# Optimization experiments

Hardware: AMD Instinct MI355X
Metric: run time of the kernel (lower is better)

The kernel has to match this reference:

```python
import jax, jax.numpy as jnp
import numpy as np

B, T_ENC, T_DEC = 64, 256, 200
MEL, R = 80, 2
ENC_DIM = 256   # must equal attention_context_dim (context = weighted sum of encoder outputs)
ATT = 256       # attention_rnn_units == attention_context_dim
DEC = 256       # decoder_rnn_units
PRE1, PRE2 = 256, 128


def _gru(x, h, wih, whh, bih, bhh):
    # torch.nn.GRUCell math; weights are (3*H, in) torch layout
    gi = x @ wih.T + bih
    gh = h @ whh.T + bhh
    i_r, i_z, i_n = jnp.split(gi, 3, axis=-1)
    h_r, h_z, h_n = jnp.split(gh, 3, axis=-1)
    r = jax.nn.sigmoid(i_r + h_r)
    z = jax.nn.sigmoid(i_z + h_z)
    n = jnp.tanh(i_n + r * h_n)
    return (1.0 - z) * n + z * h


def setup_inputs() -> dict:
    key = jax.random.key(0)
    ks = iter(jax.random.split(key, 40))
    def nrm(shape, s=0.05):
        return jax.random.normal(next(ks), shape, dtype=jnp.float32) * s
    inp = {
        "encoder_outputs": nrm((B, T_ENC, ENC_DIM), 1.0),
        "inputs": nrm((B, T_DEC, MEL * R), 1.0),
        "memory_lengths": jax.random.randint(next(ks), (B,), T_ENC // 2, T_ENC + 1),
        # prenet
        "pre_w1": nrm((PRE1, MEL * R)), "pre_b1": jnp.zeros((PRE1,), jnp.float32),
        "pre_w2": nrm((PRE2, PRE1)),    "pre_b2": jnp.zeros((PRE2,), jnp.float32),
        # memory layer (no bias)
        "mem_w": nrm((ATT, ENC_DIM)),
        # attention GRUCell: input = prenet_out(128) + context(256)
        "att_wih": nrm((3 * ATT, PRE2 + ATT)), "att_whh": nrm((3 * ATT, ATT)),
        "att_bih": jnp.zeros((3 * ATT,), jnp.float32), "att_bhh": jnp.zeros((3 * ATT,), jnp.float32),
        # Bahdanau attention: query layer (no bias) and v vector
        "q_w": nrm((ATT, ATT)), "v_w": nrm((ATT,)),
        # project_to_decoder_in
        "proj_w": nrm((DEC, ATT + ATT)), "proj_b": jnp.zeros((DEC,), jnp.float32),
        # two decoder GRUCells
        "g1_wih": nrm((3 * DEC, DEC)), "g1_whh": nrm((3 * DEC, DEC)),
        "g1_bih": jnp.zeros((3 * DEC,), jnp.float32), "g1_bhh": jnp.zeros((3 * DEC,), jnp.float32),
        "g2_wih": nrm((3 * DEC, DEC)), "g2_whh": nrm((3 * DEC, DEC)),
        "g2_bih": jnp.zeros((3 * DEC,), jnp.float32), "g2_bhh": jnp.zeros((3 * DEC,), jnp.float32),
        # output projections
        "mel_w": nrm((MEL * R, DEC + ATT)), "mel_b": jnp.zeros((MEL * R,), jnp.float32),
        "stop_w": nrm((1, DEC + ATT)),      "stop_b": jnp.zeros((1,), jnp.float32),
    }
    return inp


def reference(encoder_outputs, inputs, memory_lengths,
              pre_w1, pre_b1, pre_w2, pre_b2, mem_w,
              att_wih, att_whh, att_bih, att_bhh, q_w, v_w,
              proj_w, proj_b,
              g1_wih, g1_whh, g1_bih, g1_bhh,
              g2_wih, g2_whh, g2_bih, g2_bhh,
              mel_w, mel_b, stop_w, stop_b):
    b = encoder_outputs.shape[0]
    processed_memory = encoder_outputs @ mem_w.T                    # (B,T_enc,ATT)
    pad_mask = jnp.arange(T_ENC)[None, :] >= memory_lengths[:, None]  # True = padding

    # teacher forcing: step t consumes previous target frame (zeros at t=0)
    x_seq = jnp.concatenate([jnp.zeros((b, 1, MEL * R), inputs.dtype), inputs[:, :-1]], axis=1)
    xs = jnp.swapaxes(x_seq, 0, 1)                                  # (T_dec,B,mel*r)

    def step(carry, x):
        h_att, ctx, h1, h2 = carry
        # prenet (dropout omitted: deterministic reference)
        pre = jax.nn.relu(jax.nn.relu(x @ pre_w1.T + pre_b1) @ pre_w2.T + pre_b2)
        # attention RNN
        h_att = _gru(jnp.concatenate([pre, ctx], -1), h_att, att_wih, att_whh, att_bih, att_bhh)
        # Bahdanau alignment
        score = jnp.einsum('btd,d->bt', jnp.tanh(processed_memory + (h_att @ q_w.T)[:, None, :]), v_w)
        score = jnp.where(pad_mask, -jnp.inf, score)
        align = jax.nn.softmax(score, axis=-1)                      # (B,T_enc)
        ctx = jnp.einsum('bt,btd->bd', align, encoder_outputs)      # (B,ATT)
        # decoder stack with residuals
        d = jnp.concatenate([h_att, ctx], -1) @ proj_w.T + proj_b
        h1 = _gru(d, h1, g1_wih, g1_whh, g1_bih, g1_bhh); d = h1 + d
        h2 = _gru(d, h2, g2_wih, g2_whh, g2_bih, g2_bhh); d = h2 + d
        p = jnp.concatenate([d, ctx], -1)
        mel = p @ mel_w.T + mel_b                                   # (B,mel*r)
        stop = jax.nn.sigmoid(p @ stop_w.T + stop_b)[:, 0]          # (B,)
        return (h_att, ctx, h1, h2), (mel, align, stop)

    zeros = lambda d: jnp.zeros((b, d), encoder_outputs.dtype)
    init = (zeros(ATT), zeros(ATT), zeros(DEC), zeros(DEC))
    _, (mels, aligns, stops) = jax.lax.scan(step, init, xs)

    mel_outputs = jnp.swapaxes(mels, 0, 1)                          # (B,T_dec,mel*r)
    attn_scores = jnp.swapaxes(aligns, 0, 1)                        # (B,T_dec,T_enc)
    stop_tokens = jnp.repeat(jnp.swapaxes(stops, 0, 1), R, axis=1)  # (B,T_dec*r)
    return mel_outputs, attn_scores, stop_tokens
```

## Files before the change

### kernel.cpp

```cpp
#include <hip/hip_runtime.h>
#include <math.h>
#include <stdint.h>

#define NB   64
#define TE   256
#define TD   200
#define MR   160

typedef _Float16 h2 __attribute__((ext_vector_type(2)));

__device__ __forceinline__ float dot2f(h2 a, h2 b, float c){
  return __builtin_amdgcn_fdot2(a, b, c, false);
}
__device__ __forceinline__ h2 u2h(unsigned int u){ return __builtin_bit_cast(h2, u); }
__device__ __forceinline__ unsigned int h2u(h2 h){ return __builtin_bit_cast(unsigned int, h); }
__device__ __forceinline__ unsigned f2u(float f){ return __builtin_bit_cast(unsigned, f); }
__device__ __forceinline__ float u2f(unsigned u){ return __builtin_bit_cast(float, u); }

__device__ __forceinline__ float sigmf(float x){
  return __fdividef(1.f, 1.f + __expf(-x));
}
__device__ __forceinline__ float tanhf_(float x){
  float ax = fabsf(x);
  float e  = __expf(-2.f*ax);
  float r  = __fdividef(1.f - e, 1.f + e);
  return copysignf(r, x);
}

static constexpr size_t OFF_PM   = 0;
static constexpr size_t OFF_ENCH = 8388608;
static constexpr size_t OFF_GIP  = 16777216;
static constexpr size_t OFF_P    = 36438016;
static constexpr size_t OFF_W2   = 49545216;
static constexpr size_t OFF_W8   = 50184192;
static constexpr size_t WS_NEEDED = 52936704;

static constexpr size_t A_PW1  = 0;
static constexpr size_t A_PW2  = 20480;
static constexpr size_t A_WIHP = 36864;
static constexpr size_t A_MEMW = 86016;
static constexpr size_t A_MELW = 118784;

static constexpr size_t B_ATTC = 0;
static constexpr size_t B_ATTH = 24576;
static constexpr size_t B_G1I  = 49152;
static constexpr size_t B_G1H  = 73728;
static constexpr size_t B_G2I  = 98304;
static constexpr size_t B_G2H  = 122880;
static constexpr size_t B_PROJ = 147456;
static constexpr size_t B_QW   = 163840;

__global__ void k_conv(const float* __restrict__ src, char* __restrict__ ws,
                       unsigned off_h2, int O, int Kh, int k0, int ld){
  int i = blockIdx.x*256 + threadIdx.x;
  if (i >= O*Kh) return;
  int o = i % O, kp = i / O;
  _Float16* dst = (_Float16*)(ws + OFF_W2) + 2*((size_t)off_h2 + i);
  dst[0] = (_Float16)src[(size_t)o*ld + k0 + 2*kp    ];
  dst[1] = (_Float16)src[(size_t)o*ld + k0 + 2*kp + 1];
}

__global__ void k_conv8(const float* __restrict__ src, char* __restrict__ ws,
                        unsigned off16, int O, int Kq, int k0, int ld){
  int i = blockIdx.x*256 + threadIdx.x;
  if (i >= O*Kq) return;
  int o = i % O, kq = i / O;
  const float* s = src + (size_t)o*ld + k0 + kq*8;
  h2 p0, p1, p2, p3;
  p0.x=(_Float16)s[0]; p0.y=(_Float16)s[1];
  p1.x=(_Float16)s[2]; p1.y=(_Float16)s[3];
  p2.x=(_Float16)s[4]; p2.y=(_Float16)s[5];
  p3.x=(_Float16)s[6]; p3.y=(_Float16)s[7];
  uint4 r; r.x=h2u(p0); r.y=h2u(p1); r.z=h2u(p2); r.w=h2u(p3);
  ((uint4*)(ws + OFF_W8))[(size_t)off16 + i] = r;
}

__global__ void k_pm(const float* __restrict__ enc, char* __restrict__ ws){
  int bt = blockIdx.x;
  int j  = threadIdx.x;
  const h2* mw = (const h2*)(ws + OFF_W2) + A_MEMW;
  _Float16* pmN  = (_Float16*)(ws + OFF_PM);
  _Float16* encH = (_Float16*)(ws + OFF_ENCH);
  __shared__ _Float16 e[256];
  float ev = enc[(size_t)bt*256 + j];
  e[j] = (_Float16)ev;
  encH[(size_t)bt*256 + j] = (_Float16)ev;
  __syncthreads();
  const h2* e2 = (const h2*)e;
  float acc = 0.f;
  #pragma unroll 8
  for (int kp=0; kp<128; ++kp) acc = dot2f(mw[kp*256 + j], e2[kp], acc);
  pmN[(size_t)bt*256 + j] = (_Float16)acc;
}

__global__ void k_pre(const float* __restrict__ xin, const float* __restrict__ b1,
                      const float* __restrict__ b2, const float* __restrict__ bih,
                      char* __restrict__ ws){
  int bt = blockIdx.x;
  int b = bt / TD, t = bt % TD;
  int j = threadIdx.x;
  const h2* w1 = (const h2*)(ws + OFF_W2) + A_PW1;
  const h2* w2 = (const h2*)(ws + OFF_W2) + A_PW2;
  const h2* wp = (const h2*)(ws + OFF_W2) + A_WIHP;
  _Float16* gip = (_Float16*)(ws + OFF_GIP) + (size_t)bt*768;
  __shared__ _Float16 xh[160];
  __shared__ _Float16 a1[256];
  __shared__ _Float16 pr[128];
  if (j < 160)
    xh[j] = (t==0) ? (_Float16)0.f : (_Float16)xin[((size_t)b*TD + (t-1))*MR + j];
  __syncthreads();
  {
    const h2* x2 = (const h2*)xh;
    float acc = b1[j];
    #pragma unroll 8
    for (int kp=0; kp<80; ++kp) acc = dot2f(w1[kp*256 + j], x2[kp], acc);
    a1[j] = (_Float16)fmaxf(acc, 0.f);
  }
  __syncthreads();
  if (j < 128){
    const h2* x2 = (const h2*)a1;
    float acc = b2[j];
    #pragma unroll 8
    for (int kp=0; kp<128; ++kp) acc = dot2f(w2[kp*128 + j], x2[kp], acc);
    pr[j] = (_Float16)fmaxf(acc, 0.f);
  }
  __syncthreads();
  {
    const h2* p2 = (const h2*)pr;
    for (int o=j; o<768; o+=256){
      float acc = bih[o];
      #pragma unroll 8
      for (int kp=0; kp<64; ++kp) acc = dot2f(wp[kp*768 + o], p2[kp], acc);
      gip[o] = (_Float16)acc;
    }
  }
}

__global__ void k_zero(float* __restrict__ out){
  int* prog = (int*)(out + (size_t)NB*TD*MR + (size_t)NB*TD*TE);
  if (threadIdx.x < 256) prog[threadIdx.x] = 0;
}

__device__ __forceinline__ float d4dot(uint4 w, uint4 x, float a){
  a = dot2f(u2h(w.x), u2h(x.x), a);
  a = dot2f(u2h(w.y), u2h(x.y), a);
  a = dot2f(u2h(w.z), u2h(x.z), a);
  a = dot2f(u2h(w.w), u2h(x.w), a);
  return a;
}

__device__ __forceinline__ void gemv4(const uint4* __restrict__ wI, const uint4* __restrict__ wH,
                                      const uint4* xI, const uint4* xH,
                                      int j, int ks, float* scr, int tid){
  float a0=0.f,a1=0.f,a2=0.f,a3=0.f;
  #pragma unroll 2
  for (int kq=ks*8; kq<ks*8+8; ++kq){
    uint4 xi = xI[kq];
    uint4 xh = xH[kq];
    a0 = d4dot(wI[kq*768 +       j], xi, a0);
    a1 = d4dot(wI[kq*768 + 256 + j], xi, a1);
    a2 = d4dot(wI[kq*768 + 512 + j], xi, a2);
    a0 = d4dot(wH[kq*768 +       j], xh, a0);
    a1 = d4dot(wH[kq*768 + 256 + j], xh, a1);
    a3 = d4dot(wH[kq*768 + 512 + j], xh, a3);
  }
  float* r = scr + tid*4;
  r[0]=a0; r[1]=a1; r[2]=a2; r[3]=a3;
}

__global__ __launch_bounds__(1024) void k_dec(
    const int*   __restrict__ memlen,
    const float* __restrict__ att_bhh,
    const float* __restrict__ vw,
    const float* __restrict__ proj_b,
    const float* __restrict__ g1_bih, const float* __restrict__ g1_bhh,
    const float* __restrict__ g2_bih, const float* __restrict__ g2_bhh,
    float* __restrict__ out, char* __restrict__ ws)
{
  const int tid  = threadIdx.x;
  const int x    = blockIdx.x;
  const int y    = x >> 3;
  const int role = y & 3;
  const int b    = ((y >> 2) << 3) | (x & 7);
  const int ks   = tid >> 8;
  const int j    = tid & 255;

  const uint4* W8 = (const uint4*)(ws + OFF_W8);
  int* prog = (int*)(out + (size_t)NB*TD*MR + (size_t)NB*TD*TE);
  int* pP   = prog;
  int* pAl  = prog + 64;
  int* pD   = prog + 128;
  int* pB1  = prog + 192;
  unsigned* gX = (unsigned*)((_Float16*)(ws + OFF_GIP) + (size_t)b*TD*768);
  unsigned* uSlot = (unsigned*)out + (size_t)NB*TD*128 + (size_t)b*768;
  unsigned* aSlot = (unsigned*)out + (size_t)NB*TD*128 + (size_t)NB*768 + (size_t)b*256;

  __shared__ __align__(16) _Float16 hAh[256], ctxh[256], hh[256], dh[256];
  __shared__ float hAf[256], hf[256], df[256];
  __shared__ float qf[256], sc[256], al[256], vl[256];
  __shared__ float scr[4096];
  __shared__ float red2[4];
  __shared__ __align__(16) uint4 pmL[8192];

  if (role == 0){
    const uint4* wAH = W8 + B_ATTH;
    const uint4* wQ4 = W8 + B_QW;
    const uint4* pm4 = (const uint4*)(ws + OFF_PM) + (size_t)b*8192;
    const _Float16* gipB = (const _Float16*)(ws + OFF_GIP) + (size_t)b*TD*768;
    float* outA = out + (size_t)NB*TD*MR + (size_t)b*TD*TE;
    const int ml = memlen[b];

    for (int idx = tid; idx < 8192; idx += 1024){
      int tp = idx >> 5, g = idx & 31;
      pmL[(tp<<5) | (g ^ (tp & 7))] = pm4[idx];
    }
    if (tid < 256){ hAh[tid]=(_Float16)0.f; hAf[tid]=0.f; vl[tid]=vw[tid]; }
    __syncthreads();
    const uint4* hA4 = (const uint4*)hAh;

    #pragma unroll 1
    for (int t=0; t<TD; ++t){
      float a0=0.f, a1=0.f, a3=0.f;
      #pragma unroll 2
      for (int i=0;i<8;++i){
        int kq = ks*8+i;
        uint4 xv = hA4[kq];
        a0 = d4dot(wAH[kq*768 +       j], xv, a0);
        a1 = d4dot(wAH[kq*768 + 256 + j], xv, a1);
        a3 = d4dot(wAH[kq*768 + 512 + j], xv, a3);
      }
      { float* r = scr + tid*3; r[0]=a0; r[1]=a1; r[2]=a3; }
      if (t > 0 && tid==0){
        while (__hip_atomic_load(pP+b, __ATOMIC_RELAXED, __HIP_MEMORY_SCOPE_AGENT) < t)
          __builtin_amdgcn_s_sleep(1);
      }
      __syncthreads();
      if (tid < 256){
        const _Float16* gp = gipB + (size_t)t*768;
        float s0 = scr[tid*3+0]+scr[(256+tid)*3+0]+scr[(512+tid)*3+0]+scr[(768+tid)*3+0];
        float s1 = scr[tid*3+1]+scr[(256+tid)*3+1]+scr[(512+tid)*3+1]+scr[(768+tid)*3+1];
        float s3 = scr[tid*3+2]+scr[(256+tid)*3+2]+scr[(512+tid)*3+2]+scr[(768+tid)*3+2];
        float s2 = 0.f;
        if (t > 0){
          s0 += u2f(__hip_atomic_load(uSlot +       tid, __ATOMIC_RELAXED, __HIP_MEMORY_SCOPE_AGENT));
          s1 += u2f(__hip_atomic_load(uSlot + 256 + tid, __ATOMIC_RELAXED, __HIP_MEMORY_SCOPE_AGENT));
          s2  = u2f(__hip_atomic_load(uSlot + 512 + tid, __ATOMIC_RELAXED, __HIP_MEMORY_SCOPE_AGENT));
        }
        float r = sigmf(s0 + (float)gp[tid]     + att_bhh[tid]);
        float z = sigmf(s1 + (float)gp[256+tid] + att_bhh[256+tid]);
        float n = tanhf_(s2 + (float)gp[512+tid] + r*(s3 + att_bhh[512+tid]));
        float h = (1.f-z)*n + z*hAf[tid];
        hAf[tid]=h; hAh[tid]=(_Float16)h;
      }
      __syncthreads();
      { float a=0.f;
        #pragma unroll 2
        for (int kq=ks*8; kq<ks*8+8; ++kq)
          a = d4dot(wQ4[kq*256 + j], hA4[kq], a);
        scr[tid]=a; }
      if (tid<128)
        __hip_atomic_store(gX + (size_t)t*384 + tid, ((const unsigned*)hAh)[tid],
                           __ATOMIC_RELAXED, __HIP_MEMORY_SCOPE_AGENT);
      __syncthreads();
      if (tid<256) qf[tid] = scr[tid]+scr[256+tid]+scr[512+tid]+scr[768+tid];
      __syncthreads();
      { float s=0.f;
        #pragma unroll
        for (int i=0;i<8;++i){
          int g = ks*8 + i;
          uint4 q4 = pmL[(j<<5) | (g ^ (j&7))];
          int d0 = ks*64 + i*8;
          h2 p0=u2h(q4.x), p1=u2h(q4.y), p2=u2h(q4.z), p3=u2h(q4.w);
          s += vl[d0+0]*tanhf_((float)p0.x + qf[d0+0]);
          s += vl[d0+1]*tanhf_((float)p0.y + qf[d0+1]);
          s += vl[d0+2]*tanhf_((float)p1.x + qf[d0+2]);
          s += vl[d0+3]*tanhf_((float)p1.y + qf[d0+3]);
          s += vl[d0+4]*tanhf_((float)p2.x + qf[d0+4]);
          s += vl[d0+5]*tanhf_((float)p2.y + qf[d0+5]);
          s += vl[d0+6]*tanhf_((float)p3.x + qf[d0+6]);
          s += vl[d0+7]*tanhf_((float)p3.y + qf[d0+7]);
        }
        scr[tid]=s; }
      __syncthreads();
      if (tid<256){
        float s = scr[tid]+scr[256+tid]+scr[512+tid]+scr[768+tid];
        float e = (tid < ml) ? __expf(s) : 0.f;
        sc[tid] = e;
        float sv = e;
        #pragma unroll
        for (int o=32;o>0;o>>=1) sv += __shfl_down(sv,o,64);
        if ((tid&63)==0) red2[tid>>6]=sv;
      }
      __syncthreads();
      if (tid<256){
        float sum = red2[0]+red2[1]+red2[2]+red2[3];
        float a = sc[tid]*__fdividef(1.f,sum);
        outA[(size_t)t*TE + tid]=a;
        __hip_atomic_store(aSlot + tid, f2u(a),
                           __ATOMIC_RELAXED, __HIP_MEMORY_SCOPE_AGENT);
      }
      __syncthreads();
      if (tid==0)
        __hip_atomic_store(pAl+b, t+1, __ATOMIC_RELEASE, __HIP_MEMORY_SCOPE_AGENT);
    }
  } else if (role == 1){
    const uint4* wAC  = W8 + B_ATTC;
    const uint4* wPRJ = W8 + B_PROJ;
    const unsigned* encW = (const unsigned*)(ws + OFF_ENCH) + (size_t)b*TE*128;
    _Float16* pstB = (_Float16*)(ws + OFF_P) + (size_t)b*TD*512;
    unsigned* encL = (unsigned*)pmL;
    const uint4* hA4  = (const uint4*)hAh;
    const uint4* ctx4 = (const uint4*)ctxh;
    const int tsl = tid>>7, dp = tid&127;

    for (int idx = tid; idx < 32768; idx += 1024) encL[idx] = encW[idx];
    __syncthreads();

    #pragma unroll 1
    for (int t=0; t<TD; ++t){
      if (tid==0){
        while (__hip_atomic_load(pAl+b, __ATOMIC_RELAXED, __HIP_MEMORY_SCOPE_AGENT) < t+1)
          __builtin_amdgcn_s_sleep(1);
      }
      __syncthreads();
      if (tid<256)
        al[tid] = u2f(__hip_atomic_load(aSlot + tid, __ATOMIC_RELAXED, __HIP_MEMORY_SCOPE_AGENT));
      if (tid >= 256 && tid < 384)
        ((unsigned*)hAh)[tid-256] = __hip_atomic_load(gX + (size_t)t*384 + (tid-256),
                                                      __ATOMIC_RELAXED, __HIP_MEMORY_SCOPE_AGENT);
      __syncthreads();
      { float c0=0.f, c1=0.f;
        #pragma unroll 8
        for (int tp=tsl*32; tp<tsl*32+32; ++tp){
          float a = al[tp];
          h2 e = u2h(encL[tp*128 + dp]);
          c0 += a*(float)e.x; c1 += a*(float)e.y;
        }
        scr[tid*2]=c0; scr[tid*2+1]=c1; }
      __syncthreads();
      if (tid<128){
        float c0=0.f, c1=0.f;
        #pragma unroll
        for (int k=0;k<8;++k){ c0 += scr[(k*128+tid)*2]; c1 += scr[(k*128+tid)*2+1]; }
        h2 c; c.x=(_Float16)c0; c.y=(_Float16)c1;
        unsigned w = h2u(c);
        ((unsigned*)ctxh)[tid] = w;
        ((unsigned*)pstB)[(size_t)t*256 + 128 + tid] = w;
      }
      __syncthreads();
      { float a0=0.f, a1=0.f, a2=0.f;
        #pragma unroll 2
        for (int kq=ks*8; kq<ks*8+8; ++kq){
          uint4 xv = ctx4[kq];
          a0 = d4dot(wAC[kq*768 +       j], xv, a0);
          a1 = d4dot(wAC[kq*768 + 256 + j], xv, a1);
          a2 = d4dot(wAC[kq*768 + 512 + j], xv, a2);
        }
        float* r = scr + tid*3; r[0]=a0; r[1]=a1; r[2]=a2; }
      __syncthreads();
      if (tid<256){
        float p0 = scr[tid*3+0]+scr[(256+tid)*3+0]+scr[(512+tid)*3+0]+scr[(768+tid)*3+0];
        float p1 = scr[tid*3+1]+scr[(256+tid)*3+1]+scr[(512+tid)*3+1]+scr[(768+tid)*3+1];
        float p2 = scr[tid*3+2]+scr[(256+tid)*3+2]+scr[(512+tid)*3+2]+scr[(768+tid)*3+2];
        __hip_atomic_store(uSlot +       tid, f2u(p0), __ATOMIC_RELAXED, __HIP_MEMORY_SCOPE_AGENT);
        __hip_atomic_store(uSlot + 256 + tid, f2u(p1), __ATOMIC_RELAXED, __HIP_MEMORY_SCOPE_AGENT);
        __hip_atomic_store(uSlot + 512 + tid, f2u(p2), __ATOMIC_RELAXED, __HIP_MEMORY_SCOPE_AGENT);
      }
      __syncthreads();
      if (tid==0)
        __hip_atomic_store(pP+b, t+1, __ATOMIC_RELEASE, __HIP_MEMORY_SCOPE_AGENT);
      { float a=0.f;
        #pragma unroll 2
        for (int kq=ks*16; kq<ks*16+16; ++kq){
          uint4 xa = (kq < 32) ? hA4[kq] : ctx4[kq-32];
          a = d4dot(wPRJ[kq*256 + j], xa, a);
        }
        scr[tid]=a; }
      __syncthreads();
      if (tid<128){
        const int o0 = 2*tid, o1 = o0+1;
        float d0 = scr[o0]+scr[256+o0]+scr[512+o0]+scr[768+o0] + proj_b[o0];
        float d1 = scr[o1]+scr[256+o1]+scr[512+o1]+scr[768+o1] + proj_b[o1];
        h2 p; p.x=(_Float16)d0; p.y=(_Float16)d1;
        __hip_atomic_store(gX + (size_t)t*384 + 256 + tid, h2u(p),
                           __ATOMIC_RELAXED, __HIP_MEMORY_SCOPE_AGENT);
      }
      __syncthreads();
      if (tid==0)
        __hip_atomic_store(pD+b, t+1, __ATOMIC_RELEASE, __HIP_MEMORY_SCOPE_AGENT);
    }
  } else {
    const bool isB1 = (role == 2);
    const uint4* wI = W8 + (isB1 ? B_G1I : B_G2I);
    const uint4* wH = W8 + (isB1 ? B_G1H : B_G2H);
    const float* bih = isB1 ? g1_bih : g2_bih;
    const float* bhh = isB1 ? g1_bhh : g2_bhh;
    int* pin = isB1 ? pD : pB1;
    unsigned* oX = (unsigned*)out + (size_t)b*TD*128;
    const unsigned* inP = isB1 ? (gX + 256) : oX;
    const int instr = isB1 ? 384 : 128;
    _Float16* pstB = (_Float16*)(ws + OFF_P) + (size_t)b*TD*512;

    if (tid<256){ hh[tid]=(_Float16)0.f; hf[tid]=0.f; }
    __syncthreads();
    const uint4* h4  = (const uint4*)hh;
    const uint4* dd4 = (const uint4*)dh;

    #pragma unroll 1
    for (int t=0; t<TD; ++t){
      if (tid==0){
        while (__hip_atomic_load(pin+b, __ATOMIC_RELAXED, __HIP_MEMORY_SCOPE_AGENT) < t+1)
          __builtin_amdgcn_s_sleep(1);
      }
      __syncthreads();
      if (tid<128){
        unsigned w = __hip_atomic_load(inP + (size_t)t*instr + tid,
                                       __ATOMIC_RELAXED, __HIP_MEMORY_SCOPE_AGENT);
        ((unsigned*)dh)[tid] = w;
        h2 p = u2h(w);
        df[2*tid]   = (float)p.x;
        df[2*tid+1] = (float)p.y;
      }
      __syncthreads();
      gemv4(wI, wH, dd4, h4, j, ks, scr, tid);
      __syncthreads();
      if (tid<256){
        float s0 = scr[tid*4+0]+scr[(256+tid)*4+0]+scr[(512+tid)*4+0]+scr[(768+tid)*4+0];
        float s1 = scr[tid*4+1]+scr[(256+tid)*4+1]+scr[(512+tid)*4+1]+scr[(768+tid)*4+1];
        float s2 = scr[tid*4+2]+scr[(256+tid)*4+2]+scr[(512+tid)*4+2]+scr[(768+tid)*4+2];
        float s3 = scr[tid*4+3]+scr[(256+tid)*4+3]+scr[(512+tid)*4+3]+scr[(768+tid)*4+3];
        float r = sigmf(s0 + bih[tid]     + bhh[tid]);
        float z = sigmf(s1 + bih[256+tid] + bhh[256+tid]);
        float n = tanhf_(s2 + bih[512+tid] + r*(s3 + bhh[512+tid]));
        float h = (1.f-z)*n + z*hf[tid];
        float dn = h + df[tid];
        hf[tid]=h; hh[tid]=(_Float16)h;
        dh[tid]=(_Float16)dn;
        if (!isB1) pstB[(size_t)t*512 + tid] = (_Float16)dn;
      }
      __syncthreads();
      if (isB1){
        if (tid<128)
          __hip_atomic_store(oX + (size_t)t*128 + tid, ((const unsigned*)dh)[tid],
                             __ATOMIC_RELAXED, __HIP_MEMORY_SCOPE_AGENT);
        __syncthreads();
        if (tid==0)
          __hip_atomic_store(pB1+b, t+1, __ATOMIC_RELEASE, __HIP_MEMORY_SCOPE_AGENT);
      }
    }
  }
}

__global__ void k_post(const float* __restrict__ mel_b, const float* __restrict__ stop_w,
                       const float* __restrict__ stop_b, float* __restrict__ out,
                       char* __restrict__ ws){
  int bt = blockIdx.x;
  int b = bt / TD, t = bt % TD;
  int j = threadIdx.x;
  const h2* wm = (const h2*)(ws + OFF_W2) + A_MELW;
  const _Float16* p = (const _Float16*)(ws + OFF_P) + (size_t)bt*512;
  __shared__ _Float16 pl[512];
  ((uint32_t*)pl)[j] = ((const uint32_t*)p)[j];
  __syncthreads();
  const h2* p2 = (const h2*)pl;
  if (j < 160){
    float acc = mel_b[j];
    #pragma unroll 8
    for (int kp=0; kp<256; ++kp) acc = dot2f(wm[kp*160 + j], p2[kp], acc);
    out[(size_t)bt*MR + j] = acc;
  } else if (j == 160){
    float acc = stop_b[0];
    for (int k=0; k<512; ++k) acc += stop_w[k]*(float)pl[k];
    float s = __fdividef(1.f, 1.f + __expf(-acc));
    float* os = out + (size_t)NB*TD*MR + (size_t)NB*TD*TE + (size_t)b*2*TD;
    os[2*t]   = s;
    os[2*t+1] = s;
  }
}

extern "C" void kernel_launch(void* const* d_in, const int* in_sizes, int n_in,
                              void* d_out, int out_size, void* d_ws, size_t ws_size,
                              hipStream_t stream)
{
  const float* enc     = (const float*)d_in[0];
  const float* xin     = (const float*)d_in[1];
  const int*   mlen    = (const int*)  d_in[2];
  const float* pre_w1  = (const float*)d_in[3];
  const float* pre_b1  = (const float*)d_in[4];
  const float* pre_w2  = (const float*)d_in[5];
  const float* pre_b2  = (const float*)d_in[6];
  const float* mem_w   = (const float*)d_in[7];
  const float* att_wih = (const float*)d_in[8];
  const float* att_whh = (const float*)d_in[9];
  const float* att_bih = (const float*)d_in[10];
  const float* att_bhh = (const float*)d_in[11];
  const float* q_w     = (const float*)d_in[12];
  const float* v_w     = (const float*)d_in[13];
  const float* proj_w  = (const float*)d_in[14];
  const float* proj_b  = (const float*)d_in[15];
  const float* g1_wih  = (const float*)d_in[16];
  const float* g1_whh  = (const float*)d_in[17];
  const float* g1_bih  = (const float*)d_in[18];
  const float* g1_bhh  = (const float*)d_in[19];
  const float* g2_wih  = (const float*)d_in[20];
  const float* g2_whh  = (const float*)d_in[21];
  const float* g2_bih  = (const float*)d_in[22];
  const float* g2_bhh  = (const float*)d_in[23];
  const float* mel_w   = (const float*)d_in[24];
  const float* mel_b   = (const float*)d_in[25];
  const float* stop_w  = (const float*)d_in[26];
  const float* stop_b  = (const float*)d_in[27];
  (void)in_sizes; (void)n_in; (void)out_size;

  if (ws_size < WS_NEEDED) return;

  float* out = (float*)d_out;
  char*  ws  = (char*)d_ws;

  auto conv = [&](const float* src, size_t off_h2, int O, int Kh, int k0, int ld){
    int n = O*Kh;
    k_conv<<<(n+255)/256, 256, 0, stream>>>(src, ws, (unsigned)off_h2, O, Kh, k0, ld);
  };
  auto conv8 = [&](const float* src, size_t off16, int O, int Kq, int k0, int ld){
    int n = O*Kq;
    k_conv8<<<(n+255)/256, 256, 0, stream>>>(src, ws, (unsigned)off16, O, Kq, k0, ld);
  };

  conv(pre_w1,  A_PW1,  256, 80,  0, 160);
  conv(pre_w2,  A_PW2,  128, 128, 0, 256);
  conv(att_wih, A_WIHP, 768, 64,  0, 384);
  conv(mem_w,   A_MEMW, 256, 128, 0, 256);
  conv(mel_w,   A_MELW, 160, 256, 0, 512);
  conv8(att_wih, B_ATTC, 768, 32, 128, 384);
  conv8(att_whh, B_ATTH, 768, 32, 0,   256);
  conv8(g1_wih,  B_G1I,  768, 32, 0,   256);
  conv8(g1_whh,  B_G1H,  768, 32, 0,   256);
  conv8(g2_wih,  B_G2I,  768, 32, 0,   256);
  conv8(g2_whh,  B_G2H,  768, 32, 0,   256);
  conv8(proj_w,  B_PROJ, 256, 64, 0,   512);
  conv8(q_w,     B_QW,   256, 32, 0,   256);

  k_pm  <<<NB*TE, 256, 0, stream>>>(enc, ws);
  k_pre <<<NB*TD, 256, 0, stream>>>(xin, pre_b1, pre_b2, att_bih, ws);
  k_zero<<<1, 256, 0, stream>>>(out);
  k_dec <<<4*NB, 1024, 0, stream>>>(mlen, att_bhh, v_w, proj_b,
                                    g1_bih, g1_bhh, g2_bih, g2_bhh, out, ws);
  k_post<<<NB*TD, 256, 0, stream>>>(mel_b, stop_w, stop_b, out, ws);
}
```

Baseline: 4.463 ms.

## Reduce matvec partials with wave shuffles and defer softmax normalization to consumer

The split-K matvecs in the attention and context roles now assign the four K-slices of each output to adjacent lanes and combine them with shuffles instead of a shared-memory scratch pass, removing several barriers per step. The attention role publishes unnormalized exp scores and signals the context role before computing the softmax sum, and the context role computes the sum itself and scales the context vector. This shortens the critical path between the pipelined blocks. The trade-off is a strided weight access pattern (lanes now read rows 4 apart per kk) and duplicated reduction work.

```diff
diff --git a/kernel.cpp b/kernel.cpp
--- a/kernel.cpp
+++ b/kernel.cpp
@@ -184,6 +184,8 @@
   const int b    = ((y >> 2) << 3) | (x & 7);
   const int ks   = tid >> 8;
   const int j    = tid & 255;
+  const int jj   = tid >> 2;
+  const int kk   = tid & 3;
 
   const uint4* W8 = (const uint4*)(ws + OFF_W8);
   int* prog = (int*)(out + (size_t)NB*TD*MR + (size_t)NB*TD*TE);
@@ -196,7 +198,7 @@
   unsigned* aSlot = (unsigned*)out + (size_t)NB*TD*128 + (size_t)NB*768 + (size_t)b*256;
 
   __shared__ __align__(16) _Float16 hAh[256], ctxh[256], hh[256], dh[256];
-  __shared__ float hAf[256], hf[256], df[256];
+  __shared__ float hf[256], df[256];
   __shared__ float qf[256], sc[256], al[256], vl[256];
   __shared__ float scr[4096];
   __shared__ float red2[4];
@@ -214,62 +216,62 @@
       int tp = idx >> 5, g = idx & 31;
       pmL[(tp<<5) | (g ^ (tp & 7))] = pm4[idx];
     }
-    if (tid < 256){ hAh[tid]=(_Float16)0.f; hAf[tid]=0.f; vl[tid]=vw[tid]; }
+    if (tid < 256){ hAh[tid]=(_Float16)0.f; vl[tid]=vw[tid]; }
     __syncthreads();
     const uint4* hA4 = (const uint4*)hAh;
+    float hAprev = 0.f;
 
     #pragma unroll 1
     for (int t=0; t<TD; ++t){
       float a0=0.f, a1=0.f, a3=0.f;
       #pragma unroll 2
       for (int i=0;i<8;++i){
-        int kq = ks*8+i;
+        int kq = kk*8+i;
         uint4 xv = hA4[kq];
-        a0 = d4dot(wAH[kq*768 +       j], xv, a0);
-        a1 = d4dot(wAH[kq*768 + 256 + j], xv, a1);
-        a3 = d4dot(wAH[kq*768 + 512 + j], xv, a3);
-      }
-      { float* r = scr + tid*3; r[0]=a0; r[1]=a1; r[2]=a3; }
+        a0 = d4dot(wAH[kq*768 +       jj], xv, a0);
+        a1 = d4dot(wAH[kq*768 + 256 + jj], xv, a1);
+        a3 = d4dot(wAH[kq*768 + 512 + jj], xv, a3);
+      }
+      a0 += __shfl_down(a0,2); a0 += __shfl_down(a0,1);
+      a1 += __shfl_down(a1,2); a1 += __shfl_down(a1,1);
+      a3 += __shfl_down(a3,2); a3 += __shfl_down(a3,1);
       if (t > 0 && tid==0){
         while (__hip_atomic_load(pP+b, __ATOMIC_RELAXED, __HIP_MEMORY_SCOPE_AGENT) < t)
           __builtin_amdgcn_s_sleep(1);
       }
       __syncthreads();
-      if (tid < 256){
+      if (kk==0){
         const _Float16* gp = gipB + (size_t)t*768;
-        float s0 = scr[tid*3+0]+scr[(256+tid)*3+0]+scr[(512+tid)*3+0]+scr[(768+tid)*3+0];
-        float s1 = scr[tid*3+1]+scr[(256+tid)*3+1]+scr[(512+tid)*3+1]+scr[(768+tid)*3+1];
-        float s3 = scr[tid*3+2]+scr[(256+tid)*3+2]+scr[(512+tid)*3+2]+scr[(768+tid)*3+2];
-        float s2 = 0.f;
+        float s0=a0, s1=a1, s3=a3, s2=0.f;
         if (t > 0){
-          s0 += u2f(__hip_atomic_load(uSlot +       tid, __ATOMIC_RELAXED, __HIP_MEMORY_SCOPE_AGENT));
-          s1 += u2f(__hip_atomic_load(uSlot + 256 + tid, __ATOMIC_RELAXED, __HIP_MEMORY_SCOPE_AGENT));
-          s2  = u2f(__hip_atomic_load(uSlot + 512 + tid, __ATOMIC_RELAXED, __HIP_MEMORY_SCOPE_AGENT));
+          s0 += u2f(__hip_atomic_load(uSlot +       jj, __ATOMIC_RELAXED, __HIP_MEMORY_SCOPE_AGENT));
+          s1 += u2f(__hip_atomic_load(uSlot + 256 + jj, __ATOMIC_RELAXED, __HIP_MEMORY_SCOPE_AGENT));
+          s2  = u2f(__hip_atomic_load(uSlot + 512 + jj, __ATOMIC_RELAXED, __HIP_MEMORY_SCOPE_AGENT));
         }
-        float r = sigmf(s0 + (float)gp[tid]     + att_bhh[tid]);
-        float z = sigmf(s1 + (float)gp[256+tid] + att_bhh[256+tid]);
-        float n = tanhf_(s2 + (float)gp[512+tid] + r*(s3 + att_bhh[512+tid]));
-        float h = (1.f-z)*n + z*hAf[tid];
-        hAf[tid]=h; hAh[tid]=(_Float16)h;
+        float r = sigmf(s0 + (float)gp[jj]     + att_bhh[jj]);
+        float z = sigmf(s1 + (float)gp[256+jj] + att_bhh[256+jj]);
+        float n = tanhf_(s2 + (float)gp[512+jj] + r*(s3 + att_bhh[512+jj]));
+        float h = (1.f-z)*n + z*hAprev;
+        hAprev = h;
+        hAh[jj] = (_Float16)h;
       }
       __syncthreads();
       { float a=0.f;
         #pragma unroll 2
-        for (int kq=ks*8; kq<ks*8+8; ++kq)
-          a = d4dot(wQ4[kq*256 + j], hA4[kq], a);
-        scr[tid]=a; }
+        for (int kq=kk*8; kq<kk*8+8; ++kq)
+          a = d4dot(wQ4[kq*256 + jj], hA4[kq], a);
+        a += __shfl_down(a,2); a += __shfl_down(a,1);
+        if (kk==0) qf[jj] = a; }
       if (tid<128)
         __hip_atomic_store(gX + (size_t)t*384 + tid, ((const unsigned*)hAh)[tid],
                            __ATOMIC_RELAXED, __HIP_MEMORY_SCOPE_AGENT);
       __syncthreads();
-      if (tid<256) qf[tid] = scr[tid]+scr[256+tid]+scr[512+tid]+scr[768+tid];
-      __syncthreads();
       { float s=0.f;
         #pragma unroll
         for (int i=0;i<8;++i){
-          int g = ks*8 + i;
-          uint4 q4 = pmL[(j<<5) | (g ^ (j&7))];
-          int d0 = ks*64 + i*8;
+          int g = kk*8 + i;
+          uint4 q4 = pmL[(jj<<5) | (g ^ (jj&7))];
+          int d0 = kk*64 + i*8;
           h2 p0=u2h(q4.x), p1=u2h(q4.y), p2=u2h(q4.z), p3=u2h(q4.w);
           s += vl[d0+0]*tanhf_((float)p0.x + qf[d0+0]);
           s += vl[d0+1]*tanhf_((float)p0.y + qf[d0+1]);
@@ -280,13 +282,18 @@
           s += vl[d0+6]*tanhf_((float)p3.x + qf[d0+6]);
           s += vl[d0+7]*tanhf_((float)p3.y + qf[d0+7]);
         }
-        scr[tid]=s; }
-      __syncthreads();
+        s += __shfl_down(s,2); s += __shfl_down(s,1);
+        if (kk==0){
+          float e = (jj < ml) ? __expf(s) : 0.f;
+          sc[jj] = e;
+          __hip_atomic_store(aSlot + jj, f2u(e),
+                             __ATOMIC_RELAXED, __HIP_MEMORY_SCOPE_AGENT);
+        } }
+      __syncthreads();
+      if (tid==0)
+        __hip_atomic_store(pAl+b, t+1, __ATOMIC_RELEASE, __HIP_MEMORY_SCOPE_AGENT);
       if (tid<256){
-        float s = scr[tid]+scr[256+tid]+scr[512+tid]+scr[768+tid];
-        float e = (tid < ml) ? __expf(s) : 0.f;
-        sc[tid] = e;
-        float sv = e;
+        float sv = sc[tid];
         #pragma unroll
         for (int o=32;o>0;o>>=1) sv += __shfl_down(sv,o,64);
         if ((tid&63)==0) red2[tid>>6]=sv;
@@ -294,14 +301,8 @@
       __syncthreads();
       if (tid<256){
         float sum = red2[0]+red2[1]+red2[2]+red2[3];
-        float a = sc[tid]*__fdividef(1.f,sum);
-        outA[(size_t)t*TE + tid]=a;
-        __hip_atomic_store(aSlot + tid, f2u(a),
-                           __ATOMIC_RELAXED, __HIP_MEMORY_SCOPE_AGENT);
-      }
-      __syncthreads();
-      if (tid==0)
-        __hip_atomic_store(pAl+b, t+1, __ATOMIC_RELEASE, __HIP_MEMORY_SCOPE_AGENT);
+        outA[(size_t)t*TE + tid] = sc[tid]*__fdividef(1.f,sum);
+      }
     }
   } else if (role == 1){
     const uint4* wAC  = W8 + B_ATTC;
@@ -323,8 +324,14 @@
           __builtin_amdgcn_s_sleep(1);
       }
       __syncthreads();
-      if (tid<256)
-        al[tid] = u2f(__hip_atomic_load(aSlot + tid, __ATOMIC_RELAXED, __HIP_MEMORY_SCOPE_AGENT));
+      if (tid<256){
+        float e = u2f(__hip_atomic_load(aSlot + tid, __ATOMIC_RELAXED, __HIP_MEMORY_SCOPE_AGENT));
+        al[tid] = e;
+        float sv = e;
+        #pragma unroll
+        for (int o=32;o>0;o>>=1) sv += __shfl_down(sv,o,64);
+        if ((tid&63)==0) red2[tid>>6]=sv;
+      }
       if (tid >= 256 && tid < 384)
         ((unsigned*)hAh)[tid-256] = __hip_atomic_load(gX + (size_t)t*384 + (tid-256),
                                                       __ATOMIC_RELAXED, __HIP_MEMORY_SCOPE_AGENT);
@@ -342,7 +349,8 @@
         float c0=0.f, c1=0.f;
         #pragma unroll
         for (int k=0;k<8;++k){ c0 += scr[(k*128+tid)*2]; c1 += scr[(k*128+tid)*2+1]; }
-        h2 c; c.x=(_Float16)c0; c.y=(_Float16)c1;
+        float rs = __fdividef(1.f, red2[0]+red2[1]+red2[2]+red2[3]);
+        h2 c; c.x=(_Float16)(c0*rs); c.y=(_Float16)(c1*rs);
         unsigned w = h2u(c);
         ((unsigned*)ctxh)[tid] = w;
         ((unsigned*)pstB)[(size_t)t*256 + 128 + tid] = w;
@@ -350,22 +358,20 @@
       __syncthreads();
       { float a0=0.f, a1=0.f, a2=0.f;
         #pragma unroll 2
-        for (int kq=ks*8; kq<ks*8+8; ++kq){
+        for (int kq=kk*8; kq<kk*8+8; ++kq){
           uint4 xv = ctx4[kq];
-          a0 = d4dot(wAC[kq*768 +       j], xv, a0);
-          a1 = d4dot(wAC[kq*768 + 256 + j], xv, a1);
-          a2 = d4dot(wAC[kq*768 + 512 + j], xv, a2);
+          a0 = d4dot(wAC[kq*768 +       jj], xv, a0);
+          a1 = d4dot(wAC[kq*768 + 256 + jj], xv, a1);
+          a2 = d4dot(wAC[kq*768 + 512 + jj], xv, a2);
         }
-        float* r = scr + tid*3; r[0]=a0; r[1]=a1; r[2]=a2; }
-      __syncthreads();
-      if (tid<256){
-        float p0 = scr[tid*3+0]+scr[(256+tid)*3+0]+scr[(512+tid)*3+0]+scr[(768+tid)*3+0];
-        float p1 = scr[tid*3+1]+scr[(256+tid)*3+1]+scr[(512+tid)*3+1]+scr[(768+tid)*3+1];
-        float p2 = scr[tid*3+2]+scr[(256+tid)*3+2]+scr[(512+tid)*3+2]+scr[(768+tid)*3+2];
-        __hip_atomic_store(uSlot +       tid, f2u(p0), __ATOMIC_RELAXED, __HIP_MEMORY_SCOPE_AGENT);
-        __hip_atomic_store(uSlot + 256 + tid, f2u(p1), __ATOMIC_RELAXED, __HIP_MEMORY_SCOPE_AGENT);
-        __hip_atomic_store(uSlot + 512 + tid, f2u(p2), __ATOMIC_RELAXED, __HIP_MEMORY_SCOPE_AGENT);
-      }
+        a0 += __shfl_down(a0,2); a0 += __shfl_down(a0,1);
+        a1 += __shfl_down(a1,2); a1 += __shfl_down(a1,1);
+        a2 += __shfl_down(a2,2); a2 += __shfl_down(a2,1);
+        if (kk==0){
+          __hip_atomic_store(uSlot +       jj, f2u(a0), __ATOMIC_RELAXED, __HIP_MEMORY_SCOPE_AGENT);
+          __hip_atomic_store(uSlot + 256 + jj, f2u(a1), __ATOMIC_RELAXED, __HIP_MEMORY_SCOPE_AGENT);
+          __hip_atomic_store(uSlot + 512 + jj, f2u(a2), __ATOMIC_RELAXED, __HIP_MEMORY_SCOPE_AGENT);
+        } }
       __syncthreads();
       if (tid==0)
         __hip_atomic_store(pP+b, t+1, __ATOMIC_RELEASE, __HIP_MEMORY_SCOPE_AGENT);
```

After: 6.315 ms. +41.5%, slower.
